# Kernel optimization log

Measured on AMD Instinct MI355X. Metric: run time of the kernel, lower is better.

The kernel has to match this reference:

```python
import jax, jax.numpy as jnp
import numpy as np

N_NODES = 50000


def gcn_conv(x, W, b, src, dst, n):
    # PyG GCNConv: linear transform, add self-loops, symmetric normalization,
    # scatter-add aggregation from src -> dst, then bias.
    h = x @ W  # [N, out]
    loop = jnp.arange(n, dtype=src.dtype)
    s = jnp.concatenate([src, loop])
    d = jnp.concatenate([dst, loop])
    deg = jax.ops.segment_sum(jnp.ones(s.shape[0], dtype=h.dtype), d, num_segments=n)
    dinv = jnp.where(deg > 0, jax.lax.rsqrt(deg), 0.0)
    norm = dinv[s] * dinv[d]  # [E+N]
    msg = h[s] * norm[:, None]
    out = jax.ops.segment_sum(msg, d, num_segments=n)
    return out + b


def setup_inputs() -> dict:
    key = jax.random.key(0)
    ks = jax.random.split(key, 10)
    F_in, H, C = 256, 128, 128
    E, EL = 320000, 200000
    x = jax.random.normal(ks[0], (N_NODES, F_in), dtype=jnp.float32)
    edge_index = jax.random.randint(ks[1], (2, E), 0, N_NODES, dtype=jnp.int32)
    edge_label_index = jax.random.randint(ks[2], (2, EL), 0, N_NODES, dtype=jnp.int32)
    def glorot(k, shape):
        lim = np.sqrt(6.0 / (shape[0] + shape[1]))
        return jax.random.uniform(k, shape, jnp.float32, -lim, lim)
    W0 = glorot(ks[3], (F_in, H))
    b0 = jnp.zeros((H,), jnp.float32)
    W1 = glorot(ks[4], (H, H))
    b1 = jnp.zeros((H,), jnp.float32)
    W2 = glorot(ks[5], (H, C))
    b2 = jnp.zeros((C,), jnp.float32)
    return {"x": x, "edge_index": edge_index, "edge_label_index": edge_label_index,
            "W0": W0, "b0": b0, "W1": W1, "b1": b1, "W2": W2, "b2": b2}


def reference(x, edge_index, edge_label_index, W0, b0, W1, b1, W2, b2):
    src, dst = edge_index[0], edge_index[1]
    n = x.shape[0]
    # drop_edge keep_ratio == 1.0 -> all edges kept (deterministic)
    h = jax.nn.relu(gcn_conv(x, W0, b0, src, dst, n))
    h = jax.nn.relu(gcn_conv(h, W1, b1, src, dst, n))
    z = gcn_conv(h, W2, b2, src, dst, n)  # final conv, no activation
    # decode: dot product over candidate edge pairs
    eli = edge_label_index.astype(jnp.int32)
    logits = jnp.sum(z[eli[0]] * z[eli[1]], axis=-1)  # [E_label]
    return logits
```

## Files before the change

kernel.cpp:

```cpp
#include <hip/hip_runtime.h>
#include <hip/hip_bf16.h>


typedef __attribute__((ext_vector_type(8))) short short8v;
typedef __attribute__((ext_vector_type(4))) short short4v;
typedef __attribute__((ext_vector_type(4))) float f32x4;

__device__ inline unsigned bf16_rne(float f) {
    unsigned u = __float_as_uint(f);
    return (u + 0x7FFF + ((u >> 16) & 1)) >> 16;
}


__global__ void count_deg_kernel(const int* __restrict__ dst, int* __restrict__ deg, int E) {
    int e = blockIdx.x * blockDim.x + threadIdx.x;
    if (e < E) atomicAdd(&deg[dst[e]], 1);
}

__global__ __launch_bounds__(1024) void scan1_kernel(int* __restrict__ data,
                                                     int* __restrict__ sums, int n) {
    __shared__ int tmp[1024];
    int t = threadIdx.x;
    int idx = blockIdx.x * 1024 + t;
    int val = (idx < n) ? data[idx] : 0;
    tmp[t] = val;
    __syncthreads();
#pragma unroll
    for (int off = 1; off < 1024; off <<= 1) {
        int v = (t >= off) ? tmp[t - off] : 0;
        __syncthreads();
        tmp[t] += v;
        __syncthreads();
    }
    if (idx < n) data[idx] = tmp[t] - val;
    if (t == 1023) sums[blockIdx.x] = tmp[t];
}

__global__ void scan2_kernel(int* __restrict__ sums, int nb) {
    int lane = threadIdx.x & 63;
    int v = (lane < nb) ? sums[lane] : 0;
    int orig = v;
#pragma unroll
    for (int d = 1; d < 64; d <<= 1) {
        int t2 = __shfl_up(v, d, 64);
        if (lane >= d) v += t2;
    }
    if (lane < nb) sums[lane] = v - orig;
}

__global__ __launch_bounds__(1024) void scan3_kernel(int* __restrict__ data,
                                                     const int* __restrict__ sums, int n) {
    int idx = blockIdx.x * 1024 + threadIdx.x;
    if (idx < n && blockIdx.x > 0) data[idx] += sums[blockIdx.x];
}

__global__ void make_dinv_kernel(const int* __restrict__ off, float* __restrict__ dinv,
                                 int n, int E) {
    int v = blockIdx.x * blockDim.x + threadIdx.x;
    if (v < n) {
        int o1 = (v + 1 < n) ? off[v + 1] : E;
        float d = (float)(o1 - off[v]) + 1.0f;
        dinv[v] = 1.0f / sqrtf(d);
    }
}

__global__ void csr_fill_kernel(const int* __restrict__ src, const int* __restrict__ dst,
                                const int* __restrict__ off, int* __restrict__ fill,
                                int* __restrict__ csr_src, int E) {
    int e = blockIdx.x * blockDim.x + threadIdx.x;
    if (e >= E) return;
    int d = dst[e];
    int pos = atomicAdd(&fill[d], 1);
    csr_src[off[d] + pos] = src[e];
}


__global__ void split_w_kernel(const float* __restrict__ W, short* __restrict__ Wh,
                               short* __restrict__ Wl, int K) {
    int idx = blockIdx.x * blockDim.x + threadIdx.x;
    if (idx >= K * 128) return;
    int k = idx >> 7, col = idx & 127;
    float f = W[idx];
    unsigned h = bf16_rne(f);
    float fh = __uint_as_float(h << 16);
    unsigned l = bf16_rne(f - fh);
    Wh[col * K + k] = (short)h;
    Wl[col * K + k] = (short)l;
}


#define SWZ(row, kbyte) (((row) * 128) + ((kbyte) ^ (((row) & 7) << 4)))

__global__ __launch_bounds__(256) void gemm_mfma_kernel(const float* __restrict__ A,
                                                        const short* __restrict__ Wh_g,
                                                        const short* __restrict__ Wl_g,
                                                        float* __restrict__ out,
                                                        int M, int K) {
    __shared__ __align__(16) char smem[65536];
    char* Ah = smem;
    char* Al = smem + 16384;
    char* Bh = smem + 32768;
    char* Bl = smem + 49152;

    const int t = threadIdx.x;
    const int lane = t & 63;
    const int w = t >> 6;
    const int block_row = blockIdx.x * 128;

    f32x4 acc[2][8];
#pragma unroll
    for (int m = 0; m < 2; ++m)
#pragma unroll
        for (int c = 0; c < 8; ++c) acc[m][c] = (f32x4){0.f, 0.f, 0.f, 0.f};

    for (int k0 = 0; k0 < K; k0 += 64) {
        __syncthreads();

#pragma unroll
        for (int i = 0; i < 8; ++i) {
            int idx = t + i * 256;
            int row = idx >> 4;
            int kq  = (idx & 15) << 2;
            int grow = block_row + row;
            float4 v = make_float4(0.f, 0.f, 0.f, 0.f);
            if (grow < M) v = *reinterpret_cast<const float4*>(&A[(size_t)grow * K + k0 + kq]);
            short4v hv, lv;
            float f[4] = {v.x, v.y, v.z, v.w};
#pragma unroll
            for (int j = 0; j < 4; ++j) {
                unsigned h = bf16_rne(f[j]);
                float fh = __uint_as_float(h << 16);
                unsigned l = bf16_rne(f[j] - fh);
                hv[j] = (short)h;
                lv[j] = (short)l;
            }
            int off = SWZ(row, kq * 2);
            *reinterpret_cast<short4v*>(&Ah[off]) = hv;
            *reinterpret_cast<short4v*>(&Al[off]) = lv;
        }
#pragma unroll
        for (int i = 0; i < 4; ++i) {
            int idx = t + i * 256;
            int row = idx >> 3;
            int u   = idx & 7;
            size_t g = (size_t)row * K + k0 + u * 8;
            short8v hv = *reinterpret_cast<const short8v*>(&Wh_g[g]);
            short8v lv = *reinterpret_cast<const short8v*>(&Wl_g[g]);
            int off = SWZ(row, u * 16);
            *reinterpret_cast<short8v*>(&Bh[off]) = hv;
            *reinterpret_cast<short8v*>(&Bl[off]) = lv;
        }
        __syncthreads();

        short8v ah[2][2], al[2][2];
#pragma unroll
        for (int m = 0; m < 2; ++m)
#pragma unroll
            for (int ks = 0; ks < 2; ++ks) {
                int row = w * 32 + m * 16 + (lane & 15);
                int kb  = ks * 64 + (lane >> 4) * 16;
                ah[m][ks] = *reinterpret_cast<const short8v*>(&Ah[SWZ(row, kb)]);
                al[m][ks] = *reinterpret_cast<const short8v*>(&Al[SWZ(row, kb)]);
            }

#pragma unroll
        for (int c = 0; c < 8; ++c) {
            short8v bh[2], bl[2];
#pragma unroll
            for (int ks = 0; ks < 2; ++ks) {
                int rb = c * 16 + (lane & 15);
                int kb = ks * 64 + (lane >> 4) * 16;
                bh[ks] = *reinterpret_cast<const short8v*>(&Bh[SWZ(rb, kb)]);
                bl[ks] = *reinterpret_cast<const short8v*>(&Bl[SWZ(rb, kb)]);
            }
#pragma unroll
            for (int m = 0; m < 2; ++m)
#pragma unroll
                for (int ks = 0; ks < 2; ++ks) {
                    acc[m][c] = __builtin_amdgcn_mfma_f32_16x16x32_bf16(ah[m][ks], bh[ks], acc[m][c], 0, 0, 0);
                    acc[m][c] = __builtin_amdgcn_mfma_f32_16x16x32_bf16(ah[m][ks], bl[ks], acc[m][c], 0, 0, 0);
                    acc[m][c] = __builtin_amdgcn_mfma_f32_16x16x32_bf16(al[m][ks], bh[ks], acc[m][c], 0, 0, 0);
                }
        }
    }

#pragma unroll
    for (int m = 0; m < 2; ++m)
#pragma unroll
        for (int c = 0; c < 8; ++c)
#pragma unroll
            for (int r = 0; r < 4; ++r) {
                int row = block_row + w * 32 + m * 16 + (lane >> 4) * 4 + r;
                int col = c * 16 + (lane & 15);
                if (row < M) out[(size_t)row * 128 + col] = acc[m][c][r];
            }
}


__global__ __launch_bounds__(256) void gather_kernel(const int* __restrict__ off,
                                                     const int* __restrict__ csr_src,
                                                     const float* __restrict__ dinv,
                                                     const float* __restrict__ h,
                                                     const float* __restrict__ bias,
                                                     float* __restrict__ out,
                                                     int n, int E, int do_relu) {
    int gid = blockIdx.x * blockDim.x + threadIdx.x;
    int v = gid >> 6;
    int lane = gid & 63;
    if (v >= n) return;

    int o0 = off[v];
    int o1 = (v + 1 < n) ? off[v + 1] : E;
    float dv = dinv[v];

    float ax = 0.0f, ay = 0.0f;
    for (int j = o0; j < o1; ++j) {
        int s = csr_src[j];
        float wgt = dinv[s] * dv;
        float2 hv = *reinterpret_cast<const float2*>(&h[(size_t)s * 128 + lane * 2]);
        ax += wgt * hv.x;
        ay += wgt * hv.y;
    }
    float2 hs = *reinterpret_cast<const float2*>(&h[(size_t)v * 128 + lane * 2]);
    float2 bb = *reinterpret_cast<const float2*>(&bias[lane * 2]);
    float ox = ax + dv * dv * hs.x + bb.x;
    float oy = ay + dv * dv * hs.y + bb.y;
    if (do_relu) { ox = fmaxf(ox, 0.0f); oy = fmaxf(oy, 0.0f); }
    *reinterpret_cast<float2*>(&out[(size_t)v * 128 + lane * 2]) = make_float2(ox, oy);
}

__global__ __launch_bounds__(256) void decode_kernel(const int* __restrict__ ia,
                                                     const int* __restrict__ ib,
                                                     const float* __restrict__ z,
                                                     float* __restrict__ out, int EL) {
    int gid = blockIdx.x * blockDim.x + threadIdx.x;
    int e = gid >> 6;
    int lane = gid & 63;
    if (e >= EL) return;
    int a = ia[e], b = ib[e];
    float2 za = *reinterpret_cast<const float2*>(&z[(size_t)a * 128 + lane * 2]);
    float2 zb = *reinterpret_cast<const float2*>(&z[(size_t)b * 128 + lane * 2]);
    float s = za.x * zb.x + za.y * zb.y;
#pragma unroll
    for (int off = 32; off > 0; off >>= 1) s += __shfl_down(s, off, 64);
    if (lane == 0) out[e] = s;
}


extern "C" void kernel_launch(void* const* d_in, const int* in_sizes, int n_in,
                              void* d_out, int out_size, void* d_ws, size_t ws_size,
                              hipStream_t stream) {
    const float* x   = (const float*)d_in[0];
    const int*   ei  = (const int*)d_in[1];
    const int*   eli = (const int*)d_in[2];
    const float* W0  = (const float*)d_in[3];
    const float* b0  = (const float*)d_in[4];
    const float* W1  = (const float*)d_in[5];
    const float* b1  = (const float*)d_in[6];
    const float* W2  = (const float*)d_in[7];
    const float* b2  = (const float*)d_in[8];
    float* out = (float*)d_out;

    const int H    = in_sizes[4];
    const int F_in = in_sizes[3] / H;
    const int n    = in_sizes[0] / F_in;
    const int E    = in_sizes[1] / 2;
    const int EL   = in_sizes[2] / 2;

    const int* src = ei;
    const int* dst = ei + E;
    const int* la  = eli;
    const int* lb  = eli + EL;

    char* ws = (char*)d_ws;
    size_t p = 0;
    auto alloc = [&](size_t bytes) { char* r = ws + p; p = (p + bytes + 255) & ~(size_t)255; return r; };
    float* dinv    = (float*)alloc((size_t)n * 4);
    int*   off     = (int*)  alloc((size_t)n * 4);
    int*   csr_src = (int*)  alloc((size_t)E * 4);
    int*   sums    = (int*)  alloc(64 * 4);
    short* W0h     = (short*)alloc((size_t)F_in * H * 2);
    short* W0l     = (short*)alloc((size_t)F_in * H * 2);
    short* W1h     = (short*)alloc((size_t)H * H * 2);
    short* W1l     = (short*)alloc((size_t)H * H * 2);
    short* W2h     = (short*)alloc((size_t)H * H * 2);
    short* W2l     = (short*)alloc((size_t)H * H * 2);
    float* bufA    = (float*)alloc((size_t)n * 128 * 4);
    float* bufB    = (float*)alloc((size_t)n * 128 * 4);
    int*   fill    = (int*)bufB;

    const int T = 256;
    dim3 blk(T);

    hipMemsetAsync(off, 0, (size_t)n * 4, stream);
    hipMemsetAsync(fill, 0, (size_t)n * 4, stream);
    split_w_kernel<<<(F_in * H + T - 1) / T, blk, 0, stream>>>(W0, W0h, W0l, F_in);
    split_w_kernel<<<(H * H + T - 1) / T, blk, 0, stream>>>(W1, W1h, W1l, H);
    split_w_kernel<<<(H * H + T - 1) / T, blk, 0, stream>>>(W2, W2h, W2l, H);
    count_deg_kernel<<<(E + T - 1) / T, blk, 0, stream>>>(dst, off, E);
    int nb = (n + 1023) / 1024;
    scan1_kernel<<<nb, 1024, 0, stream>>>(off, sums, n);
    scan2_kernel<<<1, 64, 0, stream>>>(sums, nb);
    scan3_kernel<<<nb, 1024, 0, stream>>>(off, sums, n);
    make_dinv_kernel<<<(n + T - 1) / T, blk, 0, stream>>>(off, dinv, n, E);
    csr_fill_kernel<<<(E + T - 1) / T, blk, 0, stream>>>(src, dst, off, fill, csr_src, E);

    const int mblocks       = (n + 127) / 128;
    const int gather_blocks = (int)(((long long)n * 64 + T - 1) / T);

    gemm_mfma_kernel<<<mblocks, blk, 0, stream>>>(x, W0h, W0l, bufA, n, F_in);
    gather_kernel<<<gather_blocks, blk, 0, stream>>>(off, csr_src, dinv, bufA, b0, bufB, n, E, 1);

    gemm_mfma_kernel<<<mblocks, blk, 0, stream>>>(bufB, W1h, W1l, bufA, n, H);
    gather_kernel<<<gather_blocks, blk, 0, stream>>>(off, csr_src, dinv, bufA, b1, bufB, n, E, 1);

    gemm_mfma_kernel<<<mblocks, blk, 0, stream>>>(bufB, W2h, W2l, bufA, n, H);
    gather_kernel<<<gather_blocks, blk, 0, stream>>>(off, csr_src, dinv, bufA, b2, bufB, n, E, 0);

    const int dec_blocks = (int)(((long long)EL * 64 + T - 1) / T);
    decode_kernel<<<dec_blocks, blk, 0, stream>>>(la, lb, bufB, out, EL);
}
```

Baseline: 384.1 us.

## Prescale GEMM output by dinv and batch neighbor index loads in gather

The GEMM epilogue now multiplies each output row by dinv[row], so the gather no longer loads dinv[s] per edge. It only sums the prescaled rows, including the self-loop row, and multiplies by dinv[v] once at the end. The gather also loads up to 64 CSR indices cooperatively per wavefront and broadcasts them with shuffles. It unrolls by four with two accumulators so more row loads are in flight at once. Floating-point summation order changes slightly.

```diff
diff --git a/kernel.cpp b/kernel.cpp
--- a/kernel.cpp
+++ b/kernel.cpp
@@ -94,6 +94,7 @@
 __global__ __launch_bounds__(256) void gemm_mfma_kernel(const float* __restrict__ A,
                                                         const short* __restrict__ Wh_g,
                                                         const short* __restrict__ Wl_g,
+                                                        const float* __restrict__ dinv,
                                                         float* __restrict__ out,
                                                         int M, int K) {
     __shared__ __align__(16) char smem[65536];
@@ -187,20 +188,22 @@
 #pragma unroll
     for (int m = 0; m < 2; ++m)
 #pragma unroll
-        for (int c = 0; c < 8; ++c)
-#pragma unroll
-            for (int r = 0; r < 4; ++r) {
-                int row = block_row + w * 32 + m * 16 + (lane >> 4) * 4 + r;
+        for (int r = 0; r < 4; ++r) {
+            int row = block_row + w * 32 + m * 16 + (lane >> 4) * 4 + r;
+            float ds = (row < M) ? dinv[row] : 0.0f;
+#pragma unroll
+            for (int c = 0; c < 8; ++c) {
                 int col = c * 16 + (lane & 15);
-                if (row < M) out[(size_t)row * 128 + col] = acc[m][c][r];
+                if (row < M) out[(size_t)row * 128 + col] = acc[m][c][r] * ds;
             }
+        }
 }
 
 
 __global__ __launch_bounds__(256) void gather_kernel(const int* __restrict__ off,
                                                      const int* __restrict__ csr_src,
                                                      const float* __restrict__ dinv,
-                                                     const float* __restrict__ h,
+                                                     const float* __restrict__ hp,
                                                      const float* __restrict__ bias,
                                                      float* __restrict__ out,
                                                      int n, int E, int do_relu) {
@@ -211,23 +214,45 @@
 
     int o0 = off[v];
     int o1 = (v + 1 < n) ? off[v + 1] : E;
+
+    const float2* __restrict__ hp2 = reinterpret_cast<const float2*>(hp);
+    float2 sv = hp2[(size_t)v * 64 + lane];
+    float ax = sv.x, ay = sv.y;
+    float bx = 0.0f, by = 0.0f;
+
+    for (int base = o0; base < o1; base += 64) {
+        int cnt = min(64, o1 - base);
+        int myidx = (lane < cnt) ? csr_src[base + lane] : 0;
+        int j = 0;
+        for (; j + 4 <= cnt; j += 4) {
+            int i0 = __shfl(myidx, j,     64);
+            int i1 = __shfl(myidx, j + 1, 64);
+            int i2 = __shfl(myidx, j + 2, 64);
+            int i3 = __shfl(myidx, j + 3, 64);
+            float2 h0 = hp2[(size_t)i0 * 64 + lane];
+            float2 h1 = hp2[(size_t)i1 * 64 + lane];
+            float2 h2 = hp2[(size_t)i2 * 64 + lane];
+            float2 h3 = hp2[(size_t)i3 * 64 + lane];
+            ax += h0.x; ay += h0.y;
+            bx += h1.x; by += h1.y;
+            ax += h2.x; ay += h2.y;
+            bx += h3.x; by += h3.y;
+        }
+        for (; j < cnt; ++j) {
+            int s = __shfl(myidx, j, 64);
+            float2 hv = hp2[(size_t)s * 64 + lane];
+            ax += hv.x; ay += hv.y;
+        }
+    }
+
     float dv = dinv[v];
-
-    float ax = 0.0f, ay = 0.0f;
-    for (int j = o0; j < o1; ++j) {
-        int s = csr_src[j];
-        float wgt = dinv[s] * dv;
-        float2 hv = *reinterpret_cast<const float2*>(&h[(size_t)s * 128 + lane * 2]);
-        ax += wgt * hv.x;
-        ay += wgt * hv.y;
-    }
-    float2 hs = *reinterpret_cast<const float2*>(&h[(size_t)v * 128 + lane * 2]);
     float2 bb = *reinterpret_cast<const float2*>(&bias[lane * 2]);
-    float ox = ax + dv * dv * hs.x + bb.x;
-    float oy = ay + dv * dv * hs.y + bb.y;
+    float ox = dv * (ax + bx) + bb.x;
+    float oy = dv * (ay + by) + bb.y;
     if (do_relu) { ox = fmaxf(ox, 0.0f); oy = fmaxf(oy, 0.0f); }
     *reinterpret_cast<float2*>(&out[(size_t)v * 128 + lane * 2]) = make_float2(ox, oy);
 }
+
 
 __global__ __launch_bounds__(256) void decode_kernel(const int* __restrict__ ia,
                                                      const int* __restrict__ ib,
@@ -308,13 +333,13 @@
     const int mblocks       = (n + 127) / 128;
     const int gather_blocks = (int)(((long long)n * 64 + T - 1) / T);
 
-    gemm_mfma_kernel<<<mblocks, blk, 0, stream>>>(x, W0h, W0l, bufA, n, F_in);
+    gemm_mfma_kernel<<<mblocks, blk, 0, stream>>>(x, W0h, W0l, dinv, bufA, n, F_in);
     gather_kernel<<<gather_blocks, blk, 0, stream>>>(off, csr_src, dinv, bufA, b0, bufB, n, E, 1);
 
-    gemm_mfma_kernel<<<mblocks, blk, 0, stream>>>(bufB, W1h, W1l, bufA, n, H);
+    gemm_mfma_kernel<<<mblocks, blk, 0, stream>>>(bufB, W1h, W1l, dinv, bufA, n, H);
     gather_kernel<<<gather_blocks, blk, 0, stream>>>(off, csr_src, dinv, bufA, b1, bufB, n, E, 1);
 
-    gemm_mfma_kernel<<<mblocks, blk, 0, stream>>>(bufB, W2h, W2l, bufA, n, H);
+    gemm_mfma_kernel<<<mblocks, blk, 0, stream>>>(bufB, W2h, W2l, dinv, bufA, n, H);
     gather_kernel<<<gather_blocks, blk, 0, stream>>>(off, csr_src, dinv, bufA, b2, bufB, n, E, 0);
 
     const int dec_blocks = (int)(((long long)EL * 64 + T - 1) / T);
```

After: 342.7 us. 10.8% less time.
